# Kernel tuning notes

Hardware: AMD Instinct MI355X
Metric: run time of the kernel (lower is better)

## Reference

```python
import jax, jax.numpy as jnp
import numpy as np

B, LD, LQ = 32, 512, 32
E, NF = 300, 4
D = E + NF            # doc_input_size = 304
M = 16                # fofe_max_length == max_len
ALPHA = 0.9
VOCAB = 50000
H = 256
SAMPLE_NUM = 256
POS_N = 128           # int(sample_num * (1 - neg_ratio))
NEG_N = SAMPLE_NUM - POS_N
R = min(M, LD - 2)    # candidate negative lengths = 16
PPL = NEG_N // R + 1  # negatives drawn per length = 9


def setup_inputs() -> dict:
    key = jax.random.key(0)
    ks = jax.random.split(key, 16)
    emb = jax.random.normal(ks[0], (VOCAB, E), jnp.float32) * 0.1
    emb = emb.at[0].set(0.0)  # padding_idx=0
    doc = jax.random.randint(ks[1], (B, LD), 1, VOCAB)
    doc_f = jax.random.normal(ks[2], (B, LD, NF), jnp.float32) * 0.1
    query = jax.random.randint(ks[3], (B, LQ), 1, VOCAB)
    target_s = jax.random.randint(ks[4], (B,), 1, LD - M - 2)
    span = jax.random.randint(ks[5], (B,), 0, M)  # ans_span = target_e - target_s < fofe_max_length
    target_e = target_s + span
    rand_length = jax.random.permutation(ks[6], R)  # torch.randperm(min(max_len, L-2))
    # rand_position[i] ~ randint(1, LD - rand_length[i] - 1)
    u = jax.random.uniform(ks[7], (R, PPL))
    size = (LD - rand_length - 2).astype(jnp.float32)[:, None]
    rand_position = 1 + jnp.floor(u * size).astype(jnp.int32)
    rand_idx = jax.random.randint(ks[8], (NEG_N,), 0, B)  # faithful to original (dim-0 size used as bound)
    perm_idx = jax.random.permutation(ks[9], SAMPLE_NUM)

    def w(k, o, i):
        return jax.random.normal(k, (o, i), jnp.float32) * (1.0 / np.sqrt(i))

    CIN = 3 * D + E  # 1212
    W1 = w(ks[10], 4 * H, CIN)
    W2 = w(ks[11], 4 * H, 4 * H)
    W3 = w(ks[12], 4 * H, 4 * H)
    W4 = w(ks[13], 2 * H, 4 * H)
    W5 = w(ks[14], 1, 2 * H)
    doc_mask = jnp.zeros((B, LD), bool)
    query_mask = jnp.zeros((B, LQ), bool)
    return dict(doc=doc, doc_f=doc_f, query=query, target_s=target_s, target_e=target_e,
                doc_mask=doc_mask, query_mask=query_mask, emb=emb,
                W1=W1, W2=W2, W3=W3, W4=W4, W5=W5,
                rand_length=rand_length, rand_position=rand_position,
                rand_idx=rand_idx, perm_idx=perm_idx)


def _fofe_codes(x):
    """x: [B, D, LD] -> forward/inverse FOFE codes [B, D, M, LD].
    fwd[b,c,l,t] = sum_{k=0}^{l} alpha^k x[b,c,t-k]; inv mirrors to the right."""
    fwd_terms = jnp.stack(
        [(ALPHA ** k) * jnp.pad(x, ((0, 0), (0, 0), (k, 0)))[..., :LD] for k in range(M)], axis=2)
    inv_terms = jnp.stack(
        [(ALPHA ** k) * jnp.pad(x, ((0, 0), (0, 0), (0, k)))[..., k:] for k in range(M)], axis=2)
    return jnp.cumsum(fwd_terms, axis=2), jnp.cumsum(inv_terms, axis=2)


def _cnn(x, W1, W2, W3, W4, W5):
    h = jax.nn.relu(jnp.einsum('oi,bis->bos', W1, x))
    h = jax.nn.relu(jnp.einsum('oi,bis->bos', W2, h))
    h = jax.nn.relu(jnp.einsum('oi,bis->bos', W3, h))
    h = jax.nn.relu(jnp.einsum('oi,bis->bos', W4, h))
    return jax.nn.sigmoid(jnp.einsum('oi,bis->bos', W5, h))


def reference(doc, doc_f, query, target_s, target_e, doc_mask, query_mask, emb,
              W1, W2, W3, W4, W5, rand_length, rand_position, rand_idx, perm_idx):
    # input_embedding (dropout_emb = 0, pos/ner disabled)
    doc_input = jnp.concatenate([emb[doc], doc_f], axis=-1)  # [B, LD, D]
    x = jnp.swapaxes(doc_input, 1, 2)                         # [B, D, LD]
    fwd, inv = _fofe_codes(x)                                 # [B, D, M, LD] each

    # --- positive samples: gold span + left/right full contexts ---
    b = jnp.arange(B)
    span = target_e - target_s
    ans = fwd[b, :, span, target_e]                               # [B, D]
    l_ctx = fwd[b, :, M - 1, jnp.maximum(target_s - 1, 0)]        # [B, D]
    r_ctx = inv[b, :, M - 1, jnp.minimum(target_e + 1, LD - 1)]   # [B, D]
    pos = jnp.concatenate([l_ctx, ans, r_ctx], axis=-1)          # [B, 3D]
    pos = jnp.broadcast_to(pos[:, :, None], (B, 3 * D, POS_N))

    # --- negative samples: random spans of each length in rand_length ---
    rl = rand_length[:, None]                                     # [R, 1]
    neg_ans = fwd[:, :, rl, rand_position].reshape(B, D, R * PPL)
    neg_l = fwd[:, :, M - 1, rand_position - 1].reshape(B, D, R * PPL)
    neg_r = inv[:, :, M - 1, rand_position + rl + 1].reshape(B, D, R * PPL)
    rand_cat = jnp.concatenate([neg_l, neg_ans, neg_r], axis=1)   # [B, 3D, R*PPL]
    neg = rand_cat[:, :, rand_idx]                                # [B, 3D, NEG_N]

    # --- shuffle pos+neg, build query FOFE, run cnn, mse (sum) loss ---
    ctx_ans = jnp.concatenate([pos, neg], axis=-1)[:, :, perm_idx]
    target = jnp.concatenate(
        [jnp.ones((B, 1, POS_N), jnp.float32), jnp.zeros((B, 1, NEG_N), jnp.float32)],
        axis=-1)[:, :, perm_idx]
    qw = ALPHA ** jnp.arange(LQ - 1, -1, -1, dtype=jnp.float32)   # fofe_linear weights
    qf = jnp.einsum('t,bte->be', qw, emb[query])                  # [B, E]
    qb = jnp.broadcast_to(qf[:, :, None], (B, E, SAMPLE_NUM))
    dq_input = jnp.concatenate([ctx_ans, qb], axis=1)             # [B, 3D+E, S]
    score = _cnn(dq_input, W1, W2, W3, W4, W5)                    # [B, 1, S]
    loss = jnp.sum((score - target) ** 2)                         # mse_loss(size_average=False)
    return loss
```

## Files before the change

kernel.cpp:

```cpp
#include <hip/hip_runtime.h>
#include <hip/hip_bf16.h>

#define B_    32
#define LD_   512
#define LQ_   32
#define E_    300
#define NF_   4
#define D_    304
#define M_    16
#define ALPHA_ 0.9f
#define CIN_  1212
#define KP1_  1216
#define NCOL_ 1056
#define NPAD_ 1088
#define PPL_  9
#define NEG_N_ 128

typedef short short8 __attribute__((ext_vector_type(8)));
typedef float f32x4 __attribute__((ext_vector_type(4)));

__device__ __forceinline__ unsigned short f2bf(float f) {
    unsigned int x = __float_as_uint(f);
    unsigned int r = (x + 0x7FFFu + ((x >> 16) & 1u)) >> 16;
    return (unsigned short)r;
}
__device__ __forceinline__ float bf2f(unsigned short u) {
    return __uint_as_float(((unsigned int)u) << 16);
}

__global__ __launch_bounds__(128) void query_fofe(
    const int* __restrict__ query, const float* __restrict__ emb,
    unsigned short* __restrict__ qfb)
{
    int b = blockIdx.x;
    __shared__ int   rows[32];
    __shared__ float wq[32];
    int tid = threadIdx.x;
    if (tid < 32) {
        rows[tid] = query[b * LQ_ + tid];
        wq[tid] = powf(ALPHA_, (float)(LQ_ - 1 - tid));
    }
    __syncthreads();
    if (tid < 76) {
        int cc = tid * 4;
        float ax = 0.f, ay = 0.f, az = 0.f, aw = 0.f;
        if (cc < 300) {
            for (int i = 0; i < 32; ++i) {
                float4 v = *(const float4*)(emb + (size_t)rows[i] * E_ + cc);
                float wv = wq[i];
                ax += wv * v.x; ay += wv * v.y; az += wv * v.z; aw += wv * v.w;
            }
        }
        ushort4 o; o.x = f2bf(ax); o.y = f2bf(ay); o.z = f2bf(az); o.w = f2bf(aw);
        *(ushort4*)(qfb + (size_t)b * 304 + cc) = o;
    }
}

__global__ __launch_bounds__(320) void build_features(
    const int* __restrict__ doc, const float* __restrict__ doc_f,
    const int* __restrict__ target_s, const int* __restrict__ target_e,
    const float* __restrict__ emb,
    const int* __restrict__ rand_length, const int* __restrict__ rand_position,
    const unsigned short* __restrict__ qfb,
    unsigned short* __restrict__ Ft)
{
    int bcol = blockIdx.x;
    int b = bcol / 33;
    int col = bcol % 33;
    __shared__ int   s_t[3][16];
    __shared__ float s_w[3][16];
    __shared__ int   s_row[3][16];
    int tid = threadIdx.x;

    if (tid < 48) {
        int part = tid >> 4, k = tid & 15;
        int t; float valid;
        if (col == 0) {
            int ts = target_s[b], te = target_e[b];
            int span = te - ts;
            if (part == 0)      { t = ts - 1 - k;  valid = (t >= 0) ? 1.f : 0.f; }
            else if (part == 1) { t = te - k;      valid = (k <= span && t >= 0) ? 1.f : 0.f; }
            else                { t = te + 1 + k;  valid = (t < LD_) ? 1.f : 0.f; }
        } else {
            int j = col - 1;
            int r = j / PPL_, p = j - r * PPL_;
            int rl = rand_length[r];
            int rp = rand_position[r * PPL_ + p];
            if (part == 0)      { t = rp - 1 - k;      valid = (t >= 0) ? 1.f : 0.f; }
            else if (part == 1) { t = rp - k;          valid = (k <= rl && t >= 0) ? 1.f : 0.f; }
            else                { t = rp + rl + 1 + k; valid = (t < LD_) ? 1.f : 0.f; }
        }
        float w = (valid != 0.f) ? powf(ALPHA_, (float)k) : 0.f;
        t = min(max(t, 0), LD_ - 1);
        s_t[part][k] = t;
        s_w[part][k] = w;
        s_row[part][k] = doc[b * LD_ + t];
    }
    __syncthreads();

    unsigned short* out = Ft + (size_t)bcol * KP1_;
    int g = tid;
    if (g < 228) {
        int part = g / 76;
        int g2 = g - part * 76;
        int cc = g2 * 4;
        float ax = 0.f, ay = 0.f, az = 0.f, aw = 0.f;
        if (cc < 300) {
            for (int i = 0; i < 16; ++i) {
                float4 v = *(const float4*)(emb + (size_t)s_row[part][i] * E_ + cc);
                float wv = s_w[part][i];
                ax += wv * v.x; ay += wv * v.y; az += wv * v.z; aw += wv * v.w;
            }
        } else {
            for (int i = 0; i < 16; ++i) {
                float4 v = *(const float4*)(doc_f + ((size_t)b * LD_ + s_t[part][i]) * NF_);
                float wv = s_w[part][i];
                ax += wv * v.x; ay += wv * v.y; az += wv * v.z; aw += wv * v.w;
            }
        }
        ushort4 o; o.x = f2bf(ax); o.y = f2bf(ay); o.z = f2bf(az); o.w = f2bf(aw);
        *(ushort4*)(out + 4 * g) = o;
    } else if (g < 303) {
        *(ushort4*)(out + 4 * g) =
            *(const ushort4*)(qfb + (size_t)b * 304 + (g - 228) * 4);
    } else if (g == 303) {
        ushort4 z; z.x = 0; z.y = 0; z.z = 0; z.w = 0;
        *(ushort4*)(out + 4 * g) = z;
    }
}

__global__ __launch_bounds__(256) void convert_all(
    const float* __restrict__ W1, const float* __restrict__ W2,
    const float* __restrict__ W3, const float* __restrict__ W4,
    unsigned short* __restrict__ W1b, unsigned short* __restrict__ W2b,
    unsigned short* __restrict__ W3b, unsigned short* __restrict__ W4b)
{
    const long n1 = 1024L * KP1_ / 4;
    const long n2 = 1024L * 1024L / 4;
    const long n4 = 512L * 1024L / 4;
    const long total = n1 + 2 * n2 + n4;
    long stride = (long)gridDim.x * 256L;
    for (long i = (long)blockIdx.x * 256L + threadIdx.x; i < total; i += stride) {
        ushort4 o;
        if (i < n1) {
            long m = i / 304; int k4 = (int)(i - m * 304);
            if (k4 < 303) {
                float4 v = *(const float4*)(W1 + m * CIN_ + k4 * 4);
                o.x = f2bf(v.x); o.y = f2bf(v.y); o.z = f2bf(v.z); o.w = f2bf(v.w);
            } else { o.x = 0; o.y = 0; o.z = 0; o.w = 0; }
            *(ushort4*)(W1b + i * 4) = o;
        } else if (i < n1 + n2) {
            long j = i - n1;
            float4 v = *(const float4*)(W2 + j * 4);
            o.x = f2bf(v.x); o.y = f2bf(v.y); o.z = f2bf(v.z); o.w = f2bf(v.w);
            *(ushort4*)(W2b + j * 4) = o;
        } else if (i < n1 + 2 * n2) {
            long j = i - n1 - n2;
            float4 v = *(const float4*)(W3 + j * 4);
            o.x = f2bf(v.x); o.y = f2bf(v.y); o.z = f2bf(v.z); o.w = f2bf(v.w);
            *(ushort4*)(W3b + j * 4) = o;
        } else {
            long j = i - n1 - 2 * n2;
            float4 v = *(const float4*)(W4 + j * 4);
            o.x = f2bf(v.x); o.y = f2bf(v.y); o.z = f2bf(v.z); o.w = f2bf(v.w);
            *(ushort4*)(W4b + j * 4) = o;
        }
    }
}

__global__ __launch_bounds__(256) void gemm_relu(
    const unsigned short* __restrict__ A,
    const unsigned short* __restrict__ Bm,
    unsigned short* __restrict__ C,
    int M, int K)
{
    __shared__ unsigned short As[2][64][72];
    __shared__ unsigned short Bs[2][64][72];
    int tid = threadIdx.x;
    int m0 = blockIdx.x * 64, n0 = blockIdx.y * 64;
    int w = tid >> 6, lane = tid & 63;
    int wm = (w >> 1) * 32, wn = (w & 1) * 32;
    int lr = tid >> 2;
    int ls = (tid & 3) * 16;
    int fr = lane & 15, fk = (lane >> 4) * 8;

    const unsigned short* Arow = A + (size_t)(m0 + lr) * K + ls;
    const unsigned short* Brow = Bm + (size_t)(n0 + lr) * K + ls;

    f32x4 acc00 = {0.f,0.f,0.f,0.f}, acc01 = {0.f,0.f,0.f,0.f};
    f32x4 acc10 = {0.f,0.f,0.f,0.f}, acc11 = {0.f,0.f,0.f,0.f};

    int nk = K >> 6;
    {
        uint4 a0 = *(const uint4*)(Arow);
        uint4 a1 = *(const uint4*)(Arow + 8);
        uint4 b0 = *(const uint4*)(Brow);
        uint4 b1 = *(const uint4*)(Brow + 8);
        *(uint4*)&As[0][lr][ls]     = a0;
        *(uint4*)&As[0][lr][ls + 8] = a1;
        *(uint4*)&Bs[0][lr][ls]     = b0;
        *(uint4*)&Bs[0][lr][ls + 8] = b1;
    }
    __syncthreads();
    int cur = 0;
    for (int i = 0; i < nk; ++i) {
        uint4 na0, na1, nb0, nb1;
        bool more = (i + 1 < nk);
        if (more) {
            const unsigned short* An = Arow + (size_t)(i + 1) * 64;
            const unsigned short* Bn = Brow + (size_t)(i + 1) * 64;
            na0 = *(const uint4*)(An);
            na1 = *(const uint4*)(An + 8);
            nb0 = *(const uint4*)(Bn);
            nb1 = *(const uint4*)(Bn + 8);
        }
        #pragma unroll
        for (int s = 0; s < 2; ++s) {
            short8 fa0 = *(const short8*)&As[cur][wm + fr][s * 32 + fk];
            short8 fa1 = *(const short8*)&As[cur][wm + 16 + fr][s * 32 + fk];
            short8 fb0 = *(const short8*)&Bs[cur][wn + fr][s * 32 + fk];
            short8 fb1 = *(const short8*)&Bs[cur][wn + 16 + fr][s * 32 + fk];
            acc00 = __builtin_amdgcn_mfma_f32_16x16x32_bf16(fa0, fb0, acc00, 0, 0, 0);
            acc01 = __builtin_amdgcn_mfma_f32_16x16x32_bf16(fa0, fb1, acc01, 0, 0, 0);
            acc10 = __builtin_amdgcn_mfma_f32_16x16x32_bf16(fa1, fb0, acc10, 0, 0, 0);
            acc11 = __builtin_amdgcn_mfma_f32_16x16x32_bf16(fa1, fb1, acc11, 0, 0, 0);
        }
        if (more) {
            int nb = cur ^ 1;
            *(uint4*)&As[nb][lr][ls]     = na0;
            *(uint4*)&As[nb][lr][ls + 8] = na1;
            *(uint4*)&Bs[nb][lr][ls]     = nb0;
            *(uint4*)&Bs[nb][lr][ls + 8] = nb1;
        }
        __syncthreads();
        cur ^= 1;
    }

    int rbase = (lane >> 4) * 4;
    int cb = lane & 15;
    #define STORE_TILE(ACC, MT, NT) do {                                   \
        int m = m0 + wm + (MT) * 16 + rbase;                               \
        int n = n0 + wn + (NT) * 16 + cb;                                  \
        ushort4 o;                                                         \
        o.x = f2bf(fmaxf((ACC)[0], 0.f));                                  \
        o.y = f2bf(fmaxf((ACC)[1], 0.f));                                  \
        o.z = f2bf(fmaxf((ACC)[2], 0.f));                                  \
        o.w = f2bf(fmaxf((ACC)[3], 0.f));                                  \
        *(ushort4*)(C + (size_t)n * M + m) = o;                            \
    } while (0)
    STORE_TILE(acc00, 0, 0);
    STORE_TILE(acc01, 0, 1);
    STORE_TILE(acc10, 1, 0);
    STORE_TILE(acc11, 1, 1);
    #undef STORE_TILE
}

__global__ __launch_bounds__(256) void score_loss(
    const unsigned short* __restrict__ h4,
    const float* __restrict__ W5, const int* __restrict__ rand_idx,
    float* __restrict__ out)
{
    __shared__ int cnt[32];
    __shared__ float part[4];
    int tid = threadIdx.x;
    if (tid < 32) cnt[tid] = 0;
    __syncthreads();
    if (tid < NEG_N_) atomicAdd(&cnt[rand_idx[tid]], 1);
    __syncthreads();
    int w = tid >> 6, lane = tid & 63;
    int col = blockIdx.x * 4 + w;
    float v = 0.f;
    const unsigned short* row = h4 + (size_t)col * 512 + lane * 8;
    ushort4 v0 = *(const ushort4*)row;
    ushort4 v1 = *(const ushort4*)(row + 4);
    const float* w5 = W5 + lane * 8;
    float z = bf2f(v0.x) * w5[0] + bf2f(v0.y) * w5[1] +
              bf2f(v0.z) * w5[2] + bf2f(v0.w) * w5[3] +
              bf2f(v1.x) * w5[4] + bf2f(v1.y) * w5[5] +
              bf2f(v1.z) * w5[6] + bf2f(v1.w) * w5[7];
    for (int off = 32; off > 0; off >>= 1) z += __shfl_down(z, off, 64);
    if (lane == 0) {
        float s = 1.f / (1.f + expf(-z));
        int c33 = col % 33;
        if (c33 == 0) { float d = s - 1.f; v = 128.f * d * d; }
        else          { v = (float)cnt[c33 - 1] * s * s; }
        part[w] = v;
    }
    __syncthreads();
    if (tid == 0) atomicAdd(out, part[0] + part[1] + part[2] + part[3]);
}

extern "C" void kernel_launch(void* const* d_in, const int* in_sizes, int n_in,
                              void* d_out, int out_size, void* d_ws, size_t ws_size,
                              hipStream_t stream)
{
    const int*   doc        = (const int*)d_in[0];
    const float* doc_f      = (const float*)d_in[1];
    const int*   query      = (const int*)d_in[2];
    const int*   target_s   = (const int*)d_in[3];
    const int*   target_e   = (const int*)d_in[4];
    const float* emb        = (const float*)d_in[7];
    const float* W1         = (const float*)d_in[8];
    const float* W2         = (const float*)d_in[9];
    const float* W3         = (const float*)d_in[10];
    const float* W4         = (const float*)d_in[11];
    const float* W5         = (const float*)d_in[12];
    const int*   rand_length   = (const int*)d_in[13];
    const int*   rand_position = (const int*)d_in[14];
    const int*   rand_idx      = (const int*)d_in[15];

    char* ws = (char*)d_ws;
    size_t off = 0;
    auto alloc = [&](size_t bytes) {
        void* p = ws + off;
        off = (off + bytes + 255) & ~(size_t)255;
        return p;
    };
    unsigned short* W1b = (unsigned short*)alloc((size_t)1024 * KP1_ * 2);
    unsigned short* W2b = (unsigned short*)alloc((size_t)1024 * 1024 * 2);
    unsigned short* W3b = (unsigned short*)alloc((size_t)1024 * 1024 * 2);
    unsigned short* W4b = (unsigned short*)alloc((size_t)512 * 1024 * 2);
    unsigned short* Ft  = (unsigned short*)alloc((size_t)NPAD_ * KP1_ * 2);
    unsigned short* hA  = (unsigned short*)alloc((size_t)NPAD_ * 1024 * 2);
    unsigned short* hB  = (unsigned short*)alloc((size_t)NPAD_ * 1024 * 2);
    unsigned short* qfb = (unsigned short*)alloc((size_t)B_ * 304 * 2);
    float* d_loss = (float*)d_out;
    (void)ws_size; (void)in_sizes; (void)n_in; (void)out_size;

    hipMemsetAsync(Ft + (size_t)NCOL_ * KP1_, 0,
                   (size_t)(NPAD_ - NCOL_) * KP1_ * 2, stream);
    hipMemsetAsync(d_loss, 0, sizeof(float), stream);

    convert_all<<<dim3(3776), dim3(256), 0, stream>>>(W1, W2, W3, W4,
                                                      W1b, W2b, W3b, W4b);
    query_fofe<<<dim3(B_), dim3(128), 0, stream>>>(query, emb, qfb);
    build_features<<<dim3(NCOL_), dim3(320), 0, stream>>>(
        doc, doc_f, target_s, target_e, emb,
        rand_length, rand_position, qfb, Ft);

    gemm_relu<<<dim3(16, 17), dim3(256), 0, stream>>>(W1b, Ft, hA, 1024, KP1_);
    gemm_relu<<<dim3(16, 17), dim3(256), 0, stream>>>(W2b, hA, hB, 1024, 1024);
    gemm_relu<<<dim3(16, 17), dim3(256), 0, stream>>>(W3b, hB, hA, 1024, 1024);
    gemm_relu<<<dim3(8, 17),  dim3(256), 0, stream>>>(W4b, hA, hB, 512, 1024);

    score_loss<<<dim3(NCOL_ / 4), dim3(256), 0, stream>>>(hB, W5, rand_idx, d_loss);
}
```

Before: 195.1 us.

## Split the MLP GEMMs four ways along K with fp32 partials and reduce-ReLU kernels

```diff
diff --git a/kernel.cpp b/kernel.cpp
--- a/kernel.cpp
+++ b/kernel.cpp
@@ -15,6 +15,7 @@
 #define NPAD_ 1088
 #define PPL_  9
 #define NEG_N_ 128
+#define SPLITK_ 4
 
 typedef short short8 __attribute__((ext_vector_type(8)));
 typedef float f32x4 __attribute__((ext_vector_type(4)));
@@ -168,16 +169,20 @@
     }
 }
 
-__global__ __launch_bounds__(256) void gemm_relu(
+__global__ __launch_bounds__(256) void gemm_splitk(
     const unsigned short* __restrict__ A,
     const unsigned short* __restrict__ Bm,
-    unsigned short* __restrict__ C,
-    int M, int K)
+    float* __restrict__ P,
+    int M, int K, int KCI)
 {
     __shared__ unsigned short As[2][64][72];
     __shared__ unsigned short Bs[2][64][72];
     int tid = threadIdx.x;
     int m0 = blockIdx.x * 64, n0 = blockIdx.y * 64;
+    int z = blockIdx.z;
+    int nk = (K + 63) >> 6;
+    int kb = z * KCI;
+    int ke = min(nk, kb + KCI);
     int w = tid >> 6, lane = tid & 63;
     int wm = (w >> 1) * 32, wn = (w & 1) * 32;
     int lr = tid >> 2;
@@ -190,22 +195,19 @@
     f32x4 acc00 = {0.f,0.f,0.f,0.f}, acc01 = {0.f,0.f,0.f,0.f};
     f32x4 acc10 = {0.f,0.f,0.f,0.f}, acc11 = {0.f,0.f,0.f,0.f};
 
-    int nk = K >> 6;
     {
-        uint4 a0 = *(const uint4*)(Arow);
-        uint4 a1 = *(const uint4*)(Arow + 8);
-        uint4 b0 = *(const uint4*)(Brow);
-        uint4 b1 = *(const uint4*)(Brow + 8);
-        *(uint4*)&As[0][lr][ls]     = a0;
-        *(uint4*)&As[0][lr][ls + 8] = a1;
-        *(uint4*)&Bs[0][lr][ls]     = b0;
-        *(uint4*)&Bs[0][lr][ls + 8] = b1;
+        const unsigned short* An = Arow + (size_t)kb * 64;
+        const unsigned short* Bn = Brow + (size_t)kb * 64;
+        *(uint4*)&As[0][lr][ls]     = *(const uint4*)(An);
+        *(uint4*)&As[0][lr][ls + 8] = *(const uint4*)(An + 8);
+        *(uint4*)&Bs[0][lr][ls]     = *(const uint4*)(Bn);
+        *(uint4*)&Bs[0][lr][ls + 8] = *(const uint4*)(Bn + 8);
     }
     __syncthreads();
     int cur = 0;
-    for (int i = 0; i < nk; ++i) {
+    for (int i = kb; i < ke; ++i) {
         uint4 na0, na1, nb0, nb1;
-        bool more = (i + 1 < nk);
+        bool more = (i + 1 < ke);
         if (more) {
             const unsigned short* An = Arow + (size_t)(i + 1) * 64;
             const unsigned short* Bn = Brow + (size_t)(i + 1) * 64;
@@ -236,17 +238,13 @@
         cur ^= 1;
     }
 
+    float* Pz = P + (size_t)z * NPAD_ * M;
     int rbase = (lane >> 4) * 4;
     int cb = lane & 15;
     #define STORE_TILE(ACC, MT, NT) do {                                   \
         int m = m0 + wm + (MT) * 16 + rbase;                               \
         int n = n0 + wn + (NT) * 16 + cb;                                  \
-        ushort4 o;                                                         \
-        o.x = f2bf(fmaxf((ACC)[0], 0.f));                                  \
-        o.y = f2bf(fmaxf((ACC)[1], 0.f));                                  \
-        o.z = f2bf(fmaxf((ACC)[2], 0.f));                                  \
-        o.w = f2bf(fmaxf((ACC)[3], 0.f));                                  \
-        *(ushort4*)(C + (size_t)n * M + m) = o;                            \
+        *(f32x4*)(Pz + (size_t)n * M + m) = (ACC);                         \
     } while (0)
     STORE_TILE(acc00, 0, 0);
     STORE_TILE(acc01, 0, 1);
@@ -255,8 +253,25 @@
     #undef STORE_TILE
 }
 
+__global__ __launch_bounds__(256) void reduce_relu(
+    const float* __restrict__ P, unsigned short* __restrict__ out, int M)
+{
+    size_t SS = (size_t)NPAD_ * M;
+    size_t idx = ((size_t)blockIdx.x * 256 + threadIdx.x) * 4;
+    float4 a = *(const float4*)(P + idx);
+    float4 b = *(const float4*)(P + SS + idx);
+    float4 c = *(const float4*)(P + 2 * SS + idx);
+    float4 d = *(const float4*)(P + 3 * SS + idx);
+    ushort4 o;
+    o.x = f2bf(fmaxf(a.x + b.x + c.x + d.x, 0.f));
+    o.y = f2bf(fmaxf(a.y + b.y + c.y + d.y, 0.f));
+    o.z = f2bf(fmaxf(a.z + b.z + c.z + d.z, 0.f));
+    o.w = f2bf(fmaxf(a.w + b.w + c.w + d.w, 0.f));
+    *(ushort4*)(out + idx) = o;
+}
+
 __global__ __launch_bounds__(256) void score_loss(
-    const unsigned short* __restrict__ h4,
+    const float* __restrict__ P,
     const float* __restrict__ W5, const int* __restrict__ rand_idx,
     float* __restrict__ out)
 {
@@ -269,19 +284,26 @@
     __syncthreads();
     int w = tid >> 6, lane = tid & 63;
     int col = blockIdx.x * 4 + w;
-    float v = 0.f;
-    const unsigned short* row = h4 + (size_t)col * 512 + lane * 8;
-    ushort4 v0 = *(const ushort4*)row;
-    ushort4 v1 = *(const ushort4*)(row + 4);
+    const size_t SS = (size_t)NPAD_ * 512;
+    const float* row = P + (size_t)col * 512 + lane * 8;
+    float4 s0 = {0.f,0.f,0.f,0.f}, s1 = {0.f,0.f,0.f,0.f};
+    #pragma unroll
+    for (int zz = 0; zz < SPLITK_; ++zz) {
+        float4 a = *(const float4*)(row + zz * SS);
+        float4 b = *(const float4*)(row + zz * SS + 4);
+        s0.x += a.x; s0.y += a.y; s0.z += a.z; s0.w += a.w;
+        s1.x += b.x; s1.y += b.y; s1.z += b.z; s1.w += b.w;
+    }
     const float* w5 = W5 + lane * 8;
-    float z = bf2f(v0.x) * w5[0] + bf2f(v0.y) * w5[1] +
-              bf2f(v0.z) * w5[2] + bf2f(v0.w) * w5[3] +
-              bf2f(v1.x) * w5[4] + bf2f(v1.y) * w5[5] +
-              bf2f(v1.z) * w5[6] + bf2f(v1.w) * w5[7];
+    float z = fmaxf(s0.x, 0.f) * w5[0] + fmaxf(s0.y, 0.f) * w5[1] +
+              fmaxf(s0.z, 0.f) * w5[2] + fmaxf(s0.w, 0.f) * w5[3] +
+              fmaxf(s1.x, 0.f) * w5[4] + fmaxf(s1.y, 0.f) * w5[5] +
+              fmaxf(s1.z, 0.f) * w5[6] + fmaxf(s1.w, 0.f) * w5[7];
     for (int off = 32; off > 0; off >>= 1) z += __shfl_down(z, off, 64);
     if (lane == 0) {
         float s = 1.f / (1.f + expf(-z));
         int c33 = col % 33;
+        float v;
         if (c33 == 0) { float d = s - 1.f; v = 128.f * d * d; }
         else          { v = (float)cnt[c33 - 1] * s * s; }
         part[w] = v;
@@ -324,6 +346,7 @@
     unsigned short* hA  = (unsigned short*)alloc((size_t)NPAD_ * 1024 * 2);
     unsigned short* hB  = (unsigned short*)alloc((size_t)NPAD_ * 1024 * 2);
     unsigned short* qfb = (unsigned short*)alloc((size_t)B_ * 304 * 2);
+    float* P            = (float*)alloc((size_t)SPLITK_ * NPAD_ * 1024 * 4);
     float* d_loss = (float*)d_out;
     (void)ws_size; (void)in_sizes; (void)n_in; (void)out_size;
 
@@ -338,10 +361,13 @@
         doc, doc_f, target_s, target_e, emb,
         rand_length, rand_position, qfb, Ft);
 
-    gemm_relu<<<dim3(16, 17), dim3(256), 0, stream>>>(W1b, Ft, hA, 1024, KP1_);
-    gemm_relu<<<dim3(16, 17), dim3(256), 0, stream>>>(W2b, hA, hB, 1024, 1024);
-    gemm_relu<<<dim3(16, 17), dim3(256), 0, stream>>>(W3b, hB, hA, 1024, 1024);
-    gemm_relu<<<dim3(8, 17),  dim3(256), 0, stream>>>(W4b, hA, hB, 512, 1024);
-
-    score_loss<<<dim3(NCOL_ / 4), dim3(256), 0, stream>>>(hB, W5, rand_idx, d_loss);
-}
+    gemm_splitk<<<dim3(16, 17, SPLITK_), dim3(256), 0, stream>>>(W1b, Ft, P, 1024, KP1_, 5);
+    reduce_relu<<<dim3(1088), dim3(256), 0, stream>>>(P, hA, 1024);
+    gemm_splitk<<<dim3(16, 17, SPLITK_), dim3(256), 0, stream>>>(W2b, hA, P, 1024, 1024, 4);
+    reduce_relu<<<dim3(1088), dim3(256), 0, stream>>>(P, hB, 1024);
+    gemm_splitk<<<dim3(16, 17, SPLITK_), dim3(256), 0, stream>>>(W3b, hB, P, 1024, 1024, 4);
+    reduce_relu<<<dim3(1088), dim3(256), 0, stream>>>(P, hA, 1024);
+    gemm_splitk<<<dim3(8, 17, SPLITK_), dim3(256), 0, stream>>>(W4b, hA, P, 512, 1024, 4);
+
+    score_loss<<<dim3(NCOL_ / 4), dim3(256), 0, stream>>>(P, W5, rand_idx, d_loss);
+}
```

After: 207.3 us. 1.06x slower.

## Fuse whole pipeline into one persistent kernel with grid barriers

Applied to the files above, without the earlier changes.

```diff
diff --git a/kernel.cpp b/kernel.cpp
--- a/kernel.cpp
+++ b/kernel.cpp
@@ -10,11 +10,12 @@
 #define M_    16
 #define ALPHA_ 0.9f
 #define CIN_  1212
-#define KP1_  1216
+#define KP1_  1280
 #define NCOL_ 1056
 #define NPAD_ 1088
 #define PPL_  9
 #define NEG_N_ 128
+#define NB_   272
 
 typedef short short8 __attribute__((ext_vector_type(8)));
 typedef float f32x4 __attribute__((ext_vector_type(4)));
@@ -24,160 +25,41 @@
     unsigned int r = (x + 0x7FFFu + ((x >> 16) & 1u)) >> 16;
     return (unsigned short)r;
 }
-__device__ __forceinline__ float bf2f(unsigned short u) {
-    return __uint_as_float(((unsigned int)u) << 16);
-}
-
-__global__ __launch_bounds__(128) void query_fofe(
-    const int* __restrict__ query, const float* __restrict__ emb,
-    unsigned short* __restrict__ qfb)
-{
-    int b = blockIdx.x;
-    __shared__ int   rows[32];
-    __shared__ float wq[32];
-    int tid = threadIdx.x;
-    if (tid < 32) {
-        rows[tid] = query[b * LQ_ + tid];
-        wq[tid] = powf(ALPHA_, (float)(LQ_ - 1 - tid));
-    }
+
+struct GemmS { unsigned short A[2][64][72]; unsigned short B[2][64][72]; };
+union Shm {
+    GemmS g;
+    struct { int t[3][16]; float w[3][16]; int row[3][16]; } f;
+    struct { int cnt[32]; float red[256]; } l;
+};
+
+__device__ __forceinline__ void grid_barrier(unsigned* cnt, unsigned* gen, unsigned p) {
     __syncthreads();
-    if (tid < 76) {
-        int cc = tid * 4;
-        float ax = 0.f, ay = 0.f, az = 0.f, aw = 0.f;
-        if (cc < 300) {
-            for (int i = 0; i < 32; ++i) {
-                float4 v = *(const float4*)(emb + (size_t)rows[i] * E_ + cc);
-                float wv = wq[i];
-                ax += wv * v.x; ay += wv * v.y; az += wv * v.z; aw += wv * v.w;
-            }
-        }
-        ushort4 o; o.x = f2bf(ax); o.y = f2bf(ay); o.z = f2bf(az); o.w = f2bf(aw);
-        *(ushort4*)(qfb + (size_t)b * 304 + cc) = o;
-    }
-}
-
-__global__ __launch_bounds__(320) void build_features(
-    const int* __restrict__ doc, const float* __restrict__ doc_f,
-    const int* __restrict__ target_s, const int* __restrict__ target_e,
-    const float* __restrict__ emb,
-    const int* __restrict__ rand_length, const int* __restrict__ rand_position,
-    const unsigned short* __restrict__ qfb,
-    unsigned short* __restrict__ Ft)
-{
-    int bcol = blockIdx.x;
-    int b = bcol / 33;
-    int col = bcol % 33;
-    __shared__ int   s_t[3][16];
-    __shared__ float s_w[3][16];
-    __shared__ int   s_row[3][16];
-    int tid = threadIdx.x;
-
-    if (tid < 48) {
-        int part = tid >> 4, k = tid & 15;
-        int t; float valid;
-        if (col == 0) {
-            int ts = target_s[b], te = target_e[b];
-            int span = te - ts;
-            if (part == 0)      { t = ts - 1 - k;  valid = (t >= 0) ? 1.f : 0.f; }
-            else if (part == 1) { t = te - k;      valid = (k <= span && t >= 0) ? 1.f : 0.f; }
-            else                { t = te + 1 + k;  valid = (t < LD_) ? 1.f : 0.f; }
+    if (threadIdx.x == 0) {
+        __threadfence();
+        unsigned old = __hip_atomic_fetch_add(cnt, 1u, __ATOMIC_ACQ_REL,
+                                              __HIP_MEMORY_SCOPE_AGENT);
+        if (old == NB_ - 1) {
+            __hip_atomic_store(cnt, 0u, __ATOMIC_RELAXED, __HIP_MEMORY_SCOPE_AGENT);
+            __hip_atomic_fetch_add(gen, 1u, __ATOMIC_RELEASE, __HIP_MEMORY_SCOPE_AGENT);
         } else {
-            int j = col - 1;
-            int r = j / PPL_, p = j - r * PPL_;
-            int rl = rand_length[r];
-            int rp = rand_position[r * PPL_ + p];
-            if (part == 0)      { t = rp - 1 - k;      valid = (t >= 0) ? 1.f : 0.f; }
-            else if (part == 1) { t = rp - k;          valid = (k <= rl && t >= 0) ? 1.f : 0.f; }
-            else                { t = rp + rl + 1 + k; valid = (t < LD_) ? 1.f : 0.f; }
-        }
-        float w = (valid != 0.f) ? powf(ALPHA_, (float)k) : 0.f;
-        t = min(max(t, 0), LD_ - 1);
-        s_t[part][k] = t;
-        s_w[part][k] = w;
-        s_row[part][k] = doc[b * LD_ + t];
+            long spins = 0;
+            while (__hip_atomic_load(gen, __ATOMIC_ACQUIRE,
+                                     __HIP_MEMORY_SCOPE_AGENT) < p) {
+                __builtin_amdgcn_s_sleep(2);
+                if (++spins > (1L << 24)) break;
+            }
+        }
     }
     __syncthreads();
-
-    unsigned short* out = Ft + (size_t)bcol * KP1_;
-    int g = tid;
-    if (g < 228) {
-        int part = g / 76;
-        int g2 = g - part * 76;
-        int cc = g2 * 4;
-        float ax = 0.f, ay = 0.f, az = 0.f, aw = 0.f;
-        if (cc < 300) {
-            for (int i = 0; i < 16; ++i) {
-                float4 v = *(const float4*)(emb + (size_t)s_row[part][i] * E_ + cc);
-                float wv = s_w[part][i];
-                ax += wv * v.x; ay += wv * v.y; az += wv * v.z; aw += wv * v.w;
-            }
-        } else {
-            for (int i = 0; i < 16; ++i) {
-                float4 v = *(const float4*)(doc_f + ((size_t)b * LD_ + s_t[part][i]) * NF_);
-                float wv = s_w[part][i];
-                ax += wv * v.x; ay += wv * v.y; az += wv * v.z; aw += wv * v.w;
-            }
-        }
-        ushort4 o; o.x = f2bf(ax); o.y = f2bf(ay); o.z = f2bf(az); o.w = f2bf(aw);
-        *(ushort4*)(out + 4 * g) = o;
-    } else if (g < 303) {
-        *(ushort4*)(out + 4 * g) =
-            *(const ushort4*)(qfb + (size_t)b * 304 + (g - 228) * 4);
-    } else if (g == 303) {
-        ushort4 z; z.x = 0; z.y = 0; z.z = 0; z.w = 0;
-        *(ushort4*)(out + 4 * g) = z;
-    }
-}
-
-__global__ __launch_bounds__(256) void convert_all(
-    const float* __restrict__ W1, const float* __restrict__ W2,
-    const float* __restrict__ W3, const float* __restrict__ W4,
-    unsigned short* __restrict__ W1b, unsigned short* __restrict__ W2b,
-    unsigned short* __restrict__ W3b, unsigned short* __restrict__ W4b)
-{
-    const long n1 = 1024L * KP1_ / 4;
-    const long n2 = 1024L * 1024L / 4;
-    const long n4 = 512L * 1024L / 4;
-    const long total = n1 + 2 * n2 + n4;
-    long stride = (long)gridDim.x * 256L;
-    for (long i = (long)blockIdx.x * 256L + threadIdx.x; i < total; i += stride) {
-        ushort4 o;
-        if (i < n1) {
-            long m = i / 304; int k4 = (int)(i - m * 304);
-            if (k4 < 303) {
-                float4 v = *(const float4*)(W1 + m * CIN_ + k4 * 4);
-                o.x = f2bf(v.x); o.y = f2bf(v.y); o.z = f2bf(v.z); o.w = f2bf(v.w);
-            } else { o.x = 0; o.y = 0; o.z = 0; o.w = 0; }
-            *(ushort4*)(W1b + i * 4) = o;
-        } else if (i < n1 + n2) {
-            long j = i - n1;
-            float4 v = *(const float4*)(W2 + j * 4);
-            o.x = f2bf(v.x); o.y = f2bf(v.y); o.z = f2bf(v.z); o.w = f2bf(v.w);
-            *(ushort4*)(W2b + j * 4) = o;
-        } else if (i < n1 + 2 * n2) {
-            long j = i - n1 - n2;
-            float4 v = *(const float4*)(W3 + j * 4);
-            o.x = f2bf(v.x); o.y = f2bf(v.y); o.z = f2bf(v.z); o.w = f2bf(v.w);
-            *(ushort4*)(W3b + j * 4) = o;
-        } else {
-            long j = i - n1 - 2 * n2;
-            float4 v = *(const float4*)(W4 + j * 4);
-            o.x = f2bf(v.x); o.y = f2bf(v.y); o.z = f2bf(v.z); o.w = f2bf(v.w);
-            *(ushort4*)(W4b + j * 4) = o;
-        }
-    }
-}
-
-__global__ __launch_bounds__(256) void gemm_relu(
+}
+
+__device__ __forceinline__ void gemm_core(
     const unsigned short* __restrict__ A,
     const unsigned short* __restrict__ Bm,
-    unsigned short* __restrict__ C,
-    int M, int K)
+    int K, int m0, int n0, Shm& sh, f32x4 acc[4])
 {
-    __shared__ unsigned short As[2][64][72];
-    __shared__ unsigned short Bs[2][64][72];
     int tid = threadIdx.x;
-    int m0 = blockIdx.x * 64, n0 = blockIdx.y * 64;
     int w = tid >> 6, lane = tid & 63;
     int wm = (w >> 1) * 32, wn = (w & 1) * 32;
     int lr = tid >> 2;
@@ -187,20 +69,14 @@
     const unsigned short* Arow = A + (size_t)(m0 + lr) * K + ls;
     const unsigned short* Brow = Bm + (size_t)(n0 + lr) * K + ls;
 
-    f32x4 acc00 = {0.f,0.f,0.f,0.f}, acc01 = {0.f,0.f,0.f,0.f};
-    f32x4 acc10 = {0.f,0.f,0.f,0.f}, acc11 = {0.f,0.f,0.f,0.f};
+    #pragma unroll
+    for (int t = 0; t < 4; ++t) { acc[t][0]=0.f; acc[t][1]=0.f; acc[t][2]=0.f; acc[t][3]=0.f; }
 
     int nk = K >> 6;
-    {
-        uint4 a0 = *(const uint4*)(Arow);
-        uint4 a1 = *(const uint4*)(Arow + 8);
-        uint4 b0 = *(const uint4*)(Brow);
-        uint4 b1 = *(const uint4*)(Brow + 8);
-        *(uint4*)&As[0][lr][ls]     = a0;
-        *(uint4*)&As[0][lr][ls + 8] = a1;
-        *(uint4*)&Bs[0][lr][ls]     = b0;
-        *(uint4*)&Bs[0][lr][ls + 8] = b1;
-    }
+    *(uint4*)&sh.g.A[0][lr][ls]     = *(const uint4*)(Arow);
+    *(uint4*)&sh.g.A[0][lr][ls + 8] = *(const uint4*)(Arow + 8);
+    *(uint4*)&sh.g.B[0][lr][ls]     = *(const uint4*)(Brow);
+    *(uint4*)&sh.g.B[0][lr][ls + 8] = *(const uint4*)(Brow + 8);
     __syncthreads();
     int cur = 0;
     for (int i = 0; i < nk; ++i) {
@@ -216,78 +92,251 @@
         }
         #pragma unroll
         for (int s = 0; s < 2; ++s) {
-            short8 fa0 = *(const short8*)&As[cur][wm + fr][s * 32 + fk];
-            short8 fa1 = *(const short8*)&As[cur][wm + 16 + fr][s * 32 + fk];
-            short8 fb0 = *(const short8*)&Bs[cur][wn + fr][s * 32 + fk];
-            short8 fb1 = *(const short8*)&Bs[cur][wn + 16 + fr][s * 32 + fk];
-            acc00 = __builtin_amdgcn_mfma_f32_16x16x32_bf16(fa0, fb0, acc00, 0, 0, 0);
-            acc01 = __builtin_amdgcn_mfma_f32_16x16x32_bf16(fa0, fb1, acc01, 0, 0, 0);
-            acc10 = __builtin_amdgcn_mfma_f32_16x16x32_bf16(fa1, fb0, acc10, 0, 0, 0);
-            acc11 = __builtin_amdgcn_mfma_f32_16x16x32_bf16(fa1, fb1, acc11, 0, 0, 0);
+            short8 fa0 = *(const short8*)&sh.g.A[cur][wm + fr][s * 32 + fk];
+            short8 fa1 = *(const short8*)&sh.g.A[cur][wm + 16 + fr][s * 32 + fk];
+            short8 fb0 = *(const short8*)&sh.g.B[cur][wn + fr][s * 32 + fk];
+            short8 fb1 = *(const short8*)&sh.g.B[cur][wn + 16 + fr][s * 32 + fk];
+            acc[0] = __builtin_amdgcn_mfma_f32_16x16x32_bf16(fa0, fb0, acc[0], 0, 0, 0);
+            acc[1] = __builtin_amdgcn_mfma_f32_16x16x32_bf16(fa0, fb1, acc[1], 0, 0, 0);
+            acc[2] = __builtin_amdgcn_mfma_f32_16x16x32_bf16(fa1, fb0, acc[2], 0, 0, 0);
+            acc[3] = __builtin_amdgcn_mfma_f32_16x16x32_bf16(fa1, fb1, acc[3], 0, 0, 0);
         }
         if (more) {
             int nb = cur ^ 1;
-            *(uint4*)&As[nb][lr][ls]     = na0;
-            *(uint4*)&As[nb][lr][ls + 8] = na1;
-            *(uint4*)&Bs[nb][lr][ls]     = nb0;
-            *(uint4*)&Bs[nb][lr][ls + 8] = nb1;
+            *(uint4*)&sh.g.A[nb][lr][ls]     = na0;
+            *(uint4*)&sh.g.A[nb][lr][ls + 8] = na1;
+            *(uint4*)&sh.g.B[nb][lr][ls]     = nb0;
+            *(uint4*)&sh.g.B[nb][lr][ls + 8] = nb1;
         }
         __syncthreads();
         cur ^= 1;
     }
-
+}
+
+__device__ __forceinline__ void store_relu(
+    const f32x4 acc[4], unsigned short* __restrict__ C, int M, int m0, int n0)
+{
+    int tid = threadIdx.x;
+    int w = tid >> 6, lane = tid & 63;
+    int wm = (w >> 1) * 32, wn = (w & 1) * 32;
     int rbase = (lane >> 4) * 4;
     int cb = lane & 15;
-    #define STORE_TILE(ACC, MT, NT) do {                                   \
-        int m = m0 + wm + (MT) * 16 + rbase;                               \
-        int n = n0 + wn + (NT) * 16 + cb;                                  \
-        ushort4 o;                                                         \
-        o.x = f2bf(fmaxf((ACC)[0], 0.f));                                  \
-        o.y = f2bf(fmaxf((ACC)[1], 0.f));                                  \
-        o.z = f2bf(fmaxf((ACC)[2], 0.f));                                  \
-        o.w = f2bf(fmaxf((ACC)[3], 0.f));                                  \
-        *(ushort4*)(C + (size_t)n * M + m) = o;                            \
-    } while (0)
-    STORE_TILE(acc00, 0, 0);
-    STORE_TILE(acc01, 0, 1);
-    STORE_TILE(acc10, 1, 0);
-    STORE_TILE(acc11, 1, 1);
-    #undef STORE_TILE
-}
-
-__global__ __launch_bounds__(256) void score_loss(
-    const unsigned short* __restrict__ h4,
-    const float* __restrict__ W5, const int* __restrict__ rand_idx,
+    #pragma unroll
+    for (int t = 0; t < 4; ++t) {
+        int MT = t >> 1, NT = t & 1;
+        int m = m0 + wm + MT * 16 + rbase;
+        int n = n0 + wn + NT * 16 + cb;
+        ushort4 o;
+        o.x = f2bf(fmaxf(acc[t][0], 0.f));
+        o.y = f2bf(fmaxf(acc[t][1], 0.f));
+        o.z = f2bf(fmaxf(acc[t][2], 0.f));
+        o.w = f2bf(fmaxf(acc[t][3], 0.f));
+        *(ushort4*)(C + (size_t)n * M + m) = o;
+    }
+}
+
+__global__ __launch_bounds__(256, 2) void fofe_fused(
+    const int* __restrict__ doc, const float* __restrict__ doc_f,
+    const int* __restrict__ query,
+    const int* __restrict__ target_s, const int* __restrict__ target_e,
+    const float* __restrict__ emb,
+    const int* __restrict__ rand_length, const int* __restrict__ rand_position,
+    const int* __restrict__ rand_idx,
+    const float* __restrict__ W1, const float* __restrict__ W2,
+    const float* __restrict__ W3, const float* __restrict__ W4,
+    const float* __restrict__ W5,
+    unsigned short* __restrict__ W1b, unsigned short* __restrict__ W2b,
+    unsigned short* __restrict__ W3b, unsigned short* __restrict__ W4b,
+    unsigned short* __restrict__ Ft,
+    unsigned short* __restrict__ hA, unsigned short* __restrict__ hB,
+    unsigned short* __restrict__ hC,
+    float* __restrict__ zbuf, unsigned* __restrict__ bar,
     float* __restrict__ out)
 {
-    __shared__ int cnt[32];
-    __shared__ float part[4];
-    int tid = threadIdx.x;
-    if (tid < 32) cnt[tid] = 0;
-    __syncthreads();
-    if (tid < NEG_N_) atomicAdd(&cnt[rand_idx[tid]], 1);
-    __syncthreads();
-    int w = tid >> 6, lane = tid & 63;
-    int col = blockIdx.x * 4 + w;
-    float v = 0.f;
-    const unsigned short* row = h4 + (size_t)col * 512 + lane * 8;
-    ushort4 v0 = *(const ushort4*)row;
-    ushort4 v1 = *(const ushort4*)(row + 4);
-    const float* w5 = W5 + lane * 8;
-    float z = bf2f(v0.x) * w5[0] + bf2f(v0.y) * w5[1] +
-              bf2f(v0.z) * w5[2] + bf2f(v0.w) * w5[3] +
-              bf2f(v1.x) * w5[4] + bf2f(v1.y) * w5[5] +
-              bf2f(v1.z) * w5[6] + bf2f(v1.w) * w5[7];
-    for (int off = 32; off > 0; off >>= 1) z += __shfl_down(z, off, 64);
-    if (lane == 0) {
-        float s = 1.f / (1.f + expf(-z));
-        int c33 = col % 33;
-        if (c33 == 0) { float d = s - 1.f; v = 128.f * d * d; }
-        else          { v = (float)cnt[c33 - 1] * s * s; }
-        part[w] = v;
-    }
-    __syncthreads();
-    if (tid == 0) atomicAdd(out, part[0] + part[1] + part[2] + part[3]);
+    __shared__ Shm sh;
+    int bid = blockIdx.x, tid = threadIdx.x;
+    unsigned* cnt = bar;
+    unsigned* gen = bar + 1;
+
+    for (int j = 0; j < 4; ++j) {
+        int col = bid * 4 + j;
+        bool real = (col < NCOL_);
+        int b = col / 33, c33 = col % 33;
+        if (real && tid < 48) {
+            int part = tid >> 4, k = tid & 15;
+            int t; float valid;
+            if (c33 == 0) {
+                int ts = target_s[b], te = target_e[b];
+                int span = te - ts;
+                if (part == 0)      { t = ts - 1 - k;  valid = (t >= 0) ? 1.f : 0.f; }
+                else if (part == 1) { t = te - k;      valid = (k <= span && t >= 0) ? 1.f : 0.f; }
+                else                { t = te + 1 + k;  valid = (t < LD_) ? 1.f : 0.f; }
+            } else {
+                int jj = c33 - 1;
+                int r = jj / PPL_, p = jj - r * PPL_;
+                int rl = rand_length[r];
+                int rp = rand_position[r * PPL_ + p];
+                if (part == 0)      { t = rp - 1 - k;      valid = (t >= 0) ? 1.f : 0.f; }
+                else if (part == 1) { t = rp - k;          valid = (k <= rl && t >= 0) ? 1.f : 0.f; }
+                else                { t = rp + rl + 1 + k; valid = (t < LD_) ? 1.f : 0.f; }
+            }
+            float wv = (valid != 0.f) ? powf(ALPHA_, (float)k) : 0.f;
+            t = min(max(t, 0), LD_ - 1);
+            sh.f.t[part][k] = t;
+            sh.f.w[part][k] = wv;
+            sh.f.row[part][k] = doc[b * LD_ + t];
+        }
+        __syncthreads();
+        unsigned short* o4 = Ft + (size_t)col * KP1_;
+        for (int g = tid; g < 320; g += 256) {
+            ushort4 o; o.x = 0; o.y = 0; o.z = 0; o.w = 0;
+            if (real && g < 228) {
+                int part = g / 76;
+                int g2 = g - part * 76;
+                int cc = g2 * 4;
+                float ax = 0.f, ay = 0.f, az = 0.f, aw = 0.f;
+                if (cc < 300) {
+                    for (int i = 0; i < 16; ++i) {
+                        float4 v = *(const float4*)(emb + (size_t)sh.f.row[part][i] * E_ + cc);
+                        float wv = sh.f.w[part][i];
+                        ax += wv * v.x; ay += wv * v.y; az += wv * v.z; aw += wv * v.w;
+                    }
+                } else {
+                    for (int i = 0; i < 16; ++i) {
+                        float4 v = *(const float4*)(doc_f + ((size_t)b * LD_ + sh.f.t[part][i]) * NF_);
+                        float wv = sh.f.w[part][i];
+                        ax += wv * v.x; ay += wv * v.y; az += wv * v.z; aw += wv * v.w;
+                    }
+                }
+                o.x = f2bf(ax); o.y = f2bf(ay); o.z = f2bf(az); o.w = f2bf(aw);
+            } else if (real && g < 303) {
+                int ce = (g - 228) * 4;
+                float ax = 0.f, ay = 0.f, az = 0.f, aw = 0.f;
+                float wv = powf(ALPHA_, (float)(LQ_ - 1));
+                for (int i = 0; i < 32; ++i) {
+                    int row = query[b * LQ_ + i];
+                    float4 v = *(const float4*)(emb + (size_t)row * E_ + ce);
+                    ax += wv * v.x; ay += wv * v.y; az += wv * v.z; aw += wv * v.w;
+                    wv *= (1.0f / ALPHA_);
+                }
+                o.x = f2bf(ax); o.y = f2bf(ay); o.z = f2bf(az); o.w = f2bf(aw);
+            }
+            *(ushort4*)(o4 + 4 * g) = o;
+        }
+        __syncthreads();
+    }
+    if (tid < 4) zbuf[bid * 4 + tid] = 0.f;
+
+    {
+        const long n1 = 1024L * 320;
+        const long n2 = 1024L * 1024L / 4;
+        const long n4 = 512L * 1024L / 4;
+        const long total = n1 + 2 * n2 + n4;
+        const long stride = (long)NB_ * 256;
+        for (long i = (long)bid * 256 + tid; i < total; i += stride) {
+            ushort4 o;
+            if (i < n1) {
+                long m = i / 320; int k4 = (int)(i - m * 320);
+                if (k4 < 303) {
+                    float4 v = *(const float4*)(W1 + m * CIN_ + k4 * 4);
+                    o.x = f2bf(v.x); o.y = f2bf(v.y); o.z = f2bf(v.z); o.w = f2bf(v.w);
+                } else { o.x = 0; o.y = 0; o.z = 0; o.w = 0; }
+                *(ushort4*)(W1b + i * 4) = o;
+            } else if (i < n1 + n2) {
+                long jj = i - n1;
+                float4 v = *(const float4*)(W2 + jj * 4);
+                o.x = f2bf(v.x); o.y = f2bf(v.y); o.z = f2bf(v.z); o.w = f2bf(v.w);
+                *(ushort4*)(W2b + jj * 4) = o;
+            } else if (i < n1 + 2 * n2) {
+                long jj = i - n1 - n2;
+                float4 v = *(const float4*)(W3 + jj * 4);
+                o.x = f2bf(v.x); o.y = f2bf(v.y); o.z = f2bf(v.z); o.w = f2bf(v.w);
+                *(ushort4*)(W3b + jj * 4) = o;
+            } else {
+                long jj = i - n1 - 2 * n2;
+                float4 v = *(const float4*)(W4 + jj * 4);
+                o.x = f2bf(v.x); o.y = f2bf(v.y); o.z = f2bf(v.z); o.w = f2bf(v.w);
+                *(ushort4*)(W4b + jj * 4) = o;
+            }
+        }
+    }
+    grid_barrier(cnt, gen, 1);
+
+    {
+        int m0 = (bid & 15) << 6, n0 = (bid >> 4) << 6;
+        f32x4 acc[4];
+        gemm_core(W1b, Ft, KP1_, m0, n0, sh, acc);
+        store_relu(acc, hA, 1024, m0, n0);
+    }
+    grid_barrier(cnt, gen, 2);
+
+    {
+        int m0 = (bid & 15) << 6, n0 = (bid >> 4) << 6;
+        f32x4 acc[4];
+        gemm_core(W2b, hA, 1024, m0, n0, sh, acc);
+        store_relu(acc, hB, 1024, m0, n0);
+    }
+    grid_barrier(cnt, gen, 3);
+
+    {
+        int m0 = (bid & 15) << 6, n0 = (bid >> 4) << 6;
+        f32x4 acc[4];
+        gemm_core(W3b, hB, 1024, m0, n0, sh, acc);
+        store_relu(acc, hC, 1024, m0, n0);
+    }
+    grid_barrier(cnt, gen, 4);
+
+    if (bid < 136) {
+        int m0 = (bid & 7) << 6, n0 = (bid >> 3) << 6;
+        f32x4 acc[4];
+        gemm_core(W4b, hC, 1024, m0, n0, sh, acc);
+        int w = tid >> 6, lane = tid & 63;
+        int wm = (w >> 1) * 32, wn = (w & 1) * 32;
+        int fr = lane & 15, fq = lane >> 4;
+        #pragma unroll
+        for (int NT = 0; NT < 2; ++NT) {
+            float p = 0.f;
+            #pragma unroll
+            for (int MT = 0; MT < 2; ++MT) {
+                const f32x4 a = acc[MT * 2 + NT];
+                int mb = m0 + wm + MT * 16 + fq * 4;
+                p += fmaxf(a[0], 0.f) * W5[mb]
+                   + fmaxf(a[1], 0.f) * W5[mb + 1]
+                   + fmaxf(a[2], 0.f) * W5[mb + 2]
+                   + fmaxf(a[3], 0.f) * W5[mb + 3];
+            }
+            p += __shfl_down(p, 32);
+            p += __shfl_down(p, 16);
+            if (fq == 0) {
+                int n = n0 + wn + NT * 16 + fr;
+                atomicAdd(&zbuf[n], p);
+            }
+        }
+    }
+    grid_barrier(cnt, gen, 5);
+
+    if (bid == 0) {
+        if (tid < 32) sh.l.cnt[tid] = 0;
+        __syncthreads();
+        if (tid < NEG_N_) atomicAdd(&sh.l.cnt[rand_idx[tid]], 1);
+        __syncthreads();
+        float acc = 0.f;
+        for (int c = tid; c < NCOL_; c += 256) {
+            float z = __hip_atomic_load(&zbuf[c], __ATOMIC_ACQUIRE,
+                                        __HIP_MEMORY_SCOPE_AGENT);
+            float s = 1.f / (1.f + expf(-z));
+            int c33 = c % 33;
+            if (c33 == 0) { float d = s - 1.f; acc += 128.f * d * d; }
+            else          { acc += (float)sh.l.cnt[c33 - 1] * s * s; }
+        }
+        sh.l.red[tid] = acc;
+        __syncthreads();
+        for (int o = 128; o > 0; o >>= 1) {
+            if (tid < o) sh.l.red[tid] += sh.l.red[tid + o];
+            __syncthreads();
+        }
+        if (tid == 0) out[0] = sh.l.red[0];
+    }
 }
 
 extern "C" void kernel_launch(void* const* d_in, const int* in_sizes, int n_in,
@@ -323,25 +372,17 @@
     unsigned short* Ft  = (unsigned short*)alloc((size_t)NPAD_ * KP1_ * 2);
     unsigned short* hA  = (unsigned short*)alloc((size_t)NPAD_ * 1024 * 2);
     unsigned short* hB  = (unsigned short*)alloc((size_t)NPAD_ * 1024 * 2);
-    unsigned short* qfb = (unsigned short*)alloc((size_t)B_ * 304 * 2);
-    float* d_loss = (float*)d_out;
+    unsigned short* hC  = (unsigned short*)alloc((size_t)NPAD_ * 1024 * 2);
+    float*    zbuf      = (float*)alloc((size_t)NPAD_ * sizeof(float));
+    unsigned* bar       = (unsigned*)alloc(256);
     (void)ws_size; (void)in_sizes; (void)n_in; (void)out_size;
 
-    hipMemsetAsync(Ft + (size_t)NCOL_ * KP1_, 0,
-                   (size_t)(NPAD_ - NCOL_) * KP1_ * 2, stream);
-    hipMemsetAsync(d_loss, 0, sizeof(float), stream);
-
-    convert_all<<<dim3(3776), dim3(256), 0, stream>>>(W1, W2, W3, W4,
-                                                      W1b, W2b, W3b, W4b);
-    query_fofe<<<dim3(B_), dim3(128), 0, stream>>>(query, emb, qfb);
-    build_features<<<dim3(NCOL_), dim3(320), 0, stream>>>(
-        doc, doc_f, target_s, target_e, emb,
-        rand_length, rand_position, qfb, Ft);
-
-    gemm_relu<<<dim3(16, 17), dim3(256), 0, stream>>>(W1b, Ft, hA, 1024, KP1_);
-    gemm_relu<<<dim3(16, 17), dim3(256), 0, stream>>>(W2b, hA, hB, 1024, 1024);
-    gemm_relu<<<dim3(16, 17), dim3(256), 0, stream>>>(W3b, hB, hA, 1024, 1024);
-    gemm_relu<<<dim3(8, 17),  dim3(256), 0, stream>>>(W4b, hA, hB, 512, 1024);
-
-    score_loss<<<dim3(NCOL_ / 4), dim3(256), 0, stream>>>(hB, W5, rand_idx, d_loss);
-}
+    hipMemsetAsync(bar, 0, 2 * sizeof(unsigned), stream);
+
+    fofe_fused<<<dim3(NB_), dim3(256), 0, stream>>>(
+        doc, doc_f, query, target_s, target_e, emb,
+        rand_length, rand_position, rand_idx,
+        W1, W2, W3, W4, W5,
+        W1b, W2b, W3b, W4b, Ft, hA, hB, hC,
+        zbuf, bar, (float*)d_out);
+}
```

Result: slower. 538.6 us (+176.1%).
